# Kernel tuning notes

Hardware: AMD Instinct MI355X
Metric: run time of the kernel (lower is better)

The kernel has to match this reference:

```python
import jax, jax.numpy as jnp
import numpy as np

B, S, D, H = 4, 2048, 1024, 16
DK = D // H


def setup_inputs() -> dict:
    key = jax.random.key(0)
    ks = jax.random.split(key, 12)
    s = 1.0 / np.sqrt(D)
    return {
        "query": jax.random.normal(ks[0], (B, S, D), jnp.float32),
        "key": jax.random.normal(ks[1], (B, S, D), jnp.float32),
        "value": jax.random.normal(ks[2], (B, S, D), jnp.float32),
        "mask": jax.random.randint(ks[3], (B, S), 0, 2, jnp.int32),
        "wq": jax.random.normal(ks[4], (D, D), jnp.float32) * s,
        "bq": jnp.zeros((D,), jnp.float32),
        "wk": jax.random.normal(ks[5], (D, D), jnp.float32) * s,
        "bk": jnp.zeros((D,), jnp.float32),
        "wv": jax.random.normal(ks[6], (D, D), jnp.float32) * s,
        "bv": jnp.zeros((D,), jnp.float32),
        "wo": jax.random.normal(ks[7], (D, D), jnp.float32) * s,
        "bo": jnp.zeros((D,), jnp.float32),
    }


def reference(query, key, value, mask, wq, bq, wk, bk, wv, bv, wo, bo):
    # torch Linear: y = x @ W.T + b
    def proj(x, w, b):
        y = jnp.einsum('bsd,ed->bse', x, w) + b
        return y.reshape(B, S, H, DK).transpose(0, 2, 1, 3)  # [B,H,S,DK]

    q = proj(query, wq, bq)
    k = proj(key, wk, bk)
    v = proj(value, wv, bv)

    scores = jnp.einsum('bhqd,bhkd->bhqk', q, k) / jnp.sqrt(jnp.float32(DK))
    m = mask[:, None, None, :]  # [B,1,1,S_kv]
    scores = jnp.where(m == 0, jnp.float32(-1e9), scores)
    attn = jax.nn.softmax(scores, axis=-1)  # dropout p=0.0 (eval)
    out = jnp.einsum('bhqk,bhkd->bhqd', attn, v)
    out = out.transpose(0, 2, 1, 3).reshape(B, S, D)
    return jnp.einsum('bsd,ed->bse', out, wo) + bo
```

## Files before the change

kernel.cpp:

```cpp
#include <hip/hip_runtime.h>
#include <hip/hip_bf16.h>

typedef __bf16 bf16;
typedef bf16 bf16x2 __attribute__((ext_vector_type(2)));
typedef bf16 bf16x4 __attribute__((ext_vector_type(4)));
typedef bf16 bf16x8 __attribute__((ext_vector_type(8)));
typedef float f32x4 __attribute__((ext_vector_type(4)));
typedef float f32x16 __attribute__((ext_vector_type(16)));

#define MFMA16(A,B,C) __builtin_amdgcn_mfma_f32_16x16x32_bf16(A,B,C,0,0,0)
#define MFMA32(A,B,C) __builtin_amdgcn_mfma_f32_32x32x16_bf16(A,B,C,0,0,0)

__device__ __forceinline__ void gld_lds16(const void* g, void* l) {
  __builtin_amdgcn_global_load_lds(
      (const __attribute__((address_space(1))) void*)g,
      (__attribute__((address_space(3))) void*)l, 16, 0, 0);
}

__global__ void cast3_kernel(const float* __restrict__ s0, const float* __restrict__ s1,
                             const float* __restrict__ s2,
                             bf16* __restrict__ d0, bf16* __restrict__ d1, bf16* __restrict__ d2) {
  const int which = blockIdx.x >> 13;
  const int i = (blockIdx.x & 8191) * 256 + threadIdx.x;
  const float* s = which == 0 ? s0 : which == 1 ? s1 : s2;
  bf16* d = which == 0 ? d0 : which == 1 ? d1 : d2;
  float4 v = ((const float4*)s)[i];
  bf16x4 o;
  o[0] = (bf16)v.x; o[1] = (bf16)v.y; o[2] = (bf16)v.z; o[3] = (bf16)v.w;
  *(bf16x4*)(d + (size_t)i * 4) = o;
}

__global__ void cast4_kernel(const float* __restrict__ s0, const float* __restrict__ s1,
                             const float* __restrict__ s2, const float* __restrict__ s3,
                             bf16* __restrict__ d0, bf16* __restrict__ d1,
                             bf16* __restrict__ d2, bf16* __restrict__ d3) {
  const int which = blockIdx.x >> 10;
  const int i = (blockIdx.x & 1023) * 256 + threadIdx.x;
  const float* s = which == 0 ? s0 : which == 1 ? s1 : which == 2 ? s2 : s3;
  bf16* d = which == 0 ? d0 : which == 1 ? d1 : which == 2 ? d2 : d3;
  float4 v = ((const float4*)s)[i];
  bf16x4 o;
  o[0] = (bf16)v.x; o[1] = (bf16)v.y; o[2] = (bf16)v.z; o[3] = (bf16)v.w;
  *(bf16x4*)(d + (size_t)i * 4) = o;
}

template<int OUT_MODE>
__global__ __launch_bounds__(256) void gemm_bt_kernel(
    const bf16* __restrict__ A, const bf16* __restrict__ Bm,
    const float* __restrict__ bias, void* __restrict__ Cout,
    int M, int N, int K, float scale)
{
  __shared__ bf16 sA[2][128 * 32];
  __shared__ bf16 sB[2][128 * 32];
  const int t = threadIdx.x;
  const int lane = t & 63, w = t >> 6;
  const int wr = w >> 1, wc = w & 1;
  const int g = lane >> 4, c = lane & 15;
  const int bm = blockIdx.y, bn = blockIdx.x;

  f32x4 acc[4][4] = {};

  const int NT = K >> 5;
  const int arow = t >> 2;
  const int acol = (t & 3) * 8;
  const bf16* aBase = A + (size_t)(bm * 128) * K;
  const bf16* bBase = Bm + (size_t)(bn * 128) * K;

  auto stage = [&](int buf, int kt) {
    const int k0 = kt * 32;
#pragma unroll
    for (int i = 0; i < 2; ++i) {
      const int row = arow + i * 64;
      gld_lds16(aBase + (size_t)row * K + k0 + acol, &sA[buf][(i * 256 + t) * 8]);
      gld_lds16(bBase + (size_t)row * K + k0 + acol, &sB[buf][(i * 256 + t) * 8]);
    }
  };

  stage(0, 0);
  __syncthreads();
  int cur = 0;
  for (int kt = 0; kt < NT; ++kt) {
    if (kt + 1 < NT) stage(cur ^ 1, kt + 1);
    bf16x8 af[4], bfr[4];
#pragma unroll
    for (int m = 0; m < 4; ++m)
      af[m] = *(const bf16x8*)&sA[cur][(wr * 64 + m * 16 + c) * 32 + g * 8];
#pragma unroll
    for (int n = 0; n < 4; ++n)
      bfr[n] = *(const bf16x8*)&sB[cur][(wc * 64 + n * 16 + c) * 32 + g * 8];
    __builtin_amdgcn_s_setprio(1);
#pragma unroll
    for (int m = 0; m < 4; ++m)
#pragma unroll
      for (int n = 0; n < 4; ++n)
        acc[m][n] = MFMA16(af[m], bfr[n], acc[m][n]);
    __builtin_amdgcn_s_setprio(0);
    __syncthreads();
    cur ^= 1;
  }

#pragma unroll
  for (int n = 0; n < 4; ++n) {
    const int col = bn * 128 + wc * 64 + n * 16 + c;
    const float bv = bias[col];
#pragma unroll
    for (int m = 0; m < 4; ++m) {
#pragma unroll
      for (int r = 0; r < 4; ++r) {
        const int row = bm * 128 + wr * 64 + m * 16 + g * 4 + r;
        const float val = (acc[m][n][r] + bv) * scale;
        if (OUT_MODE == 0) {
          ((bf16*)Cout)[(size_t)row * N + col] = (bf16)val;
        } else if (OUT_MODE == 1) {
          const int bb = row >> 11, s = row & 2047;
          ((bf16*)Cout)[((size_t)(bb * 1024 + col)) * 2048 + s] = (bf16)val;
        } else {
          ((float*)Cout)[(size_t)row * N + col] = val;
        }
      }
    }
  }
}

__global__ __launch_bounds__(256) void attn_kernel(
    const bf16* __restrict__ Qp, const bf16* __restrict__ Kp, const bf16* __restrict__ Vt,
    const int* __restrict__ mask, bf16* __restrict__ Out)
{
  __shared__ bf16 sK[2][64 * 64];
  __shared__ bf16 sV[2][64 * 64];
  __shared__ bf16 sP[4][32 * 72];

  const int bh = blockIdx.x;
  const int b = bh >> 4, h = bh & 15;
  const int t = threadIdx.x, lane = t & 63, w = t >> 6;
  const int q32 = lane & 31, hi = lane >> 5;
  const int q0 = blockIdx.y * 128 + w * 32;

  const char* kBase = (const char*)(Kp + (size_t)(b * 2048) * 1024 + h * 64);
  const char* vBase = (const char*)(Vt + (size_t)(bh * 64) * 2048);

  auto stageKV = [&](int buf, int kt) {
#pragma unroll
    for (int i = 0; i < 2; ++i) {
      const int idx = i * 256 + t;
      const int row = idx >> 3;
      const int cb = ((t & 7) * 16) ^ ((row & 7) << 4);
      gld_lds16(kBase + (size_t)(kt * 64 + row) * 2048 + cb, (char*)sK[buf] + idx * 16);
      gld_lds16(vBase + (size_t)row * 4096 + kt * 128 + cb, (char*)sV[buf] + idx * 16);
    }
  };

  bf16x8 qf[4];
  const bf16* qrow = Qp + (size_t)(b * 2048 + q0 + q32) * 1024 + h * 64;
#pragma unroll
  for (int ks = 0; ks < 4; ++ks)
    qf[ks] = *(const bf16x8*)&qrow[ks * 16 + hi * 8];

  float mrun = -1e30f, lrun = 0.f;
  f32x16 aco[2] = {};

  const int* mrow = mask + b * 2048;
  bf16* pr = &sP[w][q32 * 72];

  stageKV(0, 0);
  __syncthreads();
  int cur = 0;
  for (int kt = 0; kt < 32; ++kt) {
    if (kt + 1 < 32) stageKV(cur ^ 1, kt + 1);

    f32x16 st[2] = {};
#pragma unroll
    for (int ks = 0; ks < 4; ++ks) {
      bf16x8 k0f, k1f;
      {
        const int row = q32;
        const int byt = (row * 128 + ks * 32 + hi * 16) ^ ((row & 7) << 4);
        k0f = *(const bf16x8*)((const char*)sK[cur] + byt);
      }
      {
        const int row = 32 + q32;
        const int byt = (row * 128 + ks * 32 + hi * 16) ^ ((row & 7) << 4);
        k1f = *(const bf16x8*)((const char*)sK[cur] + byt);
      }
      __builtin_amdgcn_s_setprio(1);
      st[0] = MFMA32(k0f, qf[ks], st[0]);
      st[1] = MFMA32(k1f, qf[ks], st[1]);
      __builtin_amdgcn_s_setprio(0);
    }

#pragma unroll
    for (int kf = 0; kf < 2; ++kf) {
#pragma unroll
      for (int q4 = 0; q4 < 4; ++q4) {
        const int4 mm = *(const int4*)&mrow[kt * 64 + kf * 32 + q4 * 8 + hi * 4];
        const int mv[4] = {mm.x, mm.y, mm.z, mm.w};
#pragma unroll
        for (int r4 = 0; r4 < 4; ++r4)
          st[kf][q4 * 4 + r4] += (mv[r4] == 0) ? -1e9f : 0.0f;
      }
    }

    float tmax = -1e30f;
#pragma unroll
    for (int i = 0; i < 16; ++i)
      tmax = fmaxf(tmax, fmaxf(st[0][i], st[1][i]));
    tmax = fmaxf(tmax, __shfl_xor(tmax, 32, 64));
    const float mnew = fmaxf(mrun, tmax);
    const float sc = exp2f(mrun - mnew);
    mrun = mnew;
    float rs = 0.f;
#pragma unroll
    for (int kf = 0; kf < 2; ++kf)
#pragma unroll
      for (int i = 0; i < 16; ++i) {
        const float p = exp2f(st[kf][i] - mnew);
        st[kf][i] = p;
        rs += p;
      }
    rs += __shfl_xor(rs, 32, 64);
    lrun = lrun * sc + rs;
    aco[0] *= sc;
    aco[1] *= sc;

#pragma unroll
    for (int kf = 0; kf < 2; ++kf)
#pragma unroll
      for (int j = 0; j < 8; ++j) {
        const int k = kf * 32 + (j >> 1) * 8 + hi * 4 + (j & 1) * 2;
        bf16x2 pv;
        pv[0] = (bf16)st[kf][2 * j];
        pv[1] = (bf16)st[kf][2 * j + 1];
        *(bf16x2*)&pr[k] = pv;
      }

    bf16x8 pa[4];
#pragma unroll
    for (int kk = 0; kk < 4; ++kk)
      pa[kk] = *(const bf16x8*)&sP[w][q32 * 72 + kk * 16 + hi * 8];
#pragma unroll
    for (int kk = 0; kk < 4; ++kk) {
      bf16x8 vb0, vb1;
      {
        const int row = q32;
        const int byt = (row * 128 + kk * 32 + hi * 16) ^ ((row & 7) << 4);
        vb0 = *(const bf16x8*)((const char*)sV[cur] + byt);
      }
      {
        const int row = 32 + q32;
        const int byt = (row * 128 + kk * 32 + hi * 16) ^ ((row & 7) << 4);
        vb1 = *(const bf16x8*)((const char*)sV[cur] + byt);
      }
      __builtin_amdgcn_s_setprio(1);
      aco[0] = MFMA32(vb0, pa[kk], aco[0]);
      aco[1] = MFMA32(vb1, pa[kk], aco[1]);
      __builtin_amdgcn_s_setprio(0);
    }

    __syncthreads();
    cur ^= 1;
  }

  const float inv = 1.0f / lrun;
  bf16* orow = Out + (size_t)(b * 2048 + q0 + q32) * 1024 + h * 64;
#pragma unroll
  for (int dkf = 0; dkf < 2; ++dkf)
#pragma unroll
    for (int q4 = 0; q4 < 4; ++q4) {
      bf16x4 o;
#pragma unroll
      for (int r4 = 0; r4 < 4; ++r4)
        o[r4] = (bf16)(aco[dkf][q4 * 4 + r4] * inv);
      *(bf16x4*)&orow[dkf * 32 + q4 * 8 + hi * 4] = o;
    }
}

extern "C" void kernel_launch(void* const* d_in, const int* in_sizes, int n_in,
                              void* d_out, int out_size, void* d_ws, size_t ws_size,
                              hipStream_t stream) {
  const float* q  = (const float*)d_in[0];
  const float* k  = (const float*)d_in[1];
  const float* v  = (const float*)d_in[2];
  const int*  msk = (const int*)d_in[3];
  const float* wq = (const float*)d_in[4];
  const float* bq = (const float*)d_in[5];
  const float* wk = (const float*)d_in[6];
  const float* bk = (const float*)d_in[7];
  const float* wv = (const float*)d_in[8];
  const float* bv = (const float*)d_in[9];
  const float* wo = (const float*)d_in[10];
  const float* bo = (const float*)d_in[11];

  bf16* ws = (bf16*)d_ws;
  const size_t NEL = 8192ull * 1024ull;
  bf16* qx  = ws;
  bf16* kx  = ws + NEL;
  bf16* vx  = ws + 2 * NEL;
  bf16* wqb = ws + 3 * NEL;
  bf16* wkb = wqb + 1048576;
  bf16* wvb = wkb + 1048576;
  bf16* wob = wvb + 1048576;
  bf16* qp  = wob + 1048576;
  bf16* kp  = qp + NEL;
  bf16* vt  = kp + NEL;
  bf16* ao  = vx;

  cast3_kernel<<<24576, 256, 0, stream>>>(q, k, v, qx, kx, vx);
  cast4_kernel<<<4096, 256, 0, stream>>>(wq, wk, wv, wo, wqb, wkb, wvb, wob);

  const float qscale = 0.125f * 1.44269504088896f;
  dim3 gg(8, 64);
  gemm_bt_kernel<0><<<gg, 256, 0, stream>>>(qx, wqb, bq, qp, 8192, 1024, 1024, qscale);
  gemm_bt_kernel<0><<<gg, 256, 0, stream>>>(kx, wkb, bk, kp, 8192, 1024, 1024, 1.0f);
  gemm_bt_kernel<1><<<gg, 256, 0, stream>>>(vx, wvb, bv, vt, 8192, 1024, 1024, 1.0f);
  attn_kernel<<<dim3(64, 16), 256, 0, stream>>>(qp, kp, vt, msk, ao);
  gemm_bt_kernel<2><<<gg, 256, 0, stream>>>(ao, wob, bo, d_out, 8192, 1024, 1024, 1.0f);
}
```

Baseline: 478.9 us.

## Keep softmax probabilities in registers via permlane swap; lazy rescale; preload mask bias

Replaces the LDS round-trip for the P tile with packed bf16 conversion and v_permlane32_swap to build the MFMA A operand directly in registers. It also initializes the score accumulator with the mask bias so the MFMA adds it, skips the running-max rescale when no new max exceeds the old one by a threshold, and splits the max and sum reductions into independent chains for more ILP. Together these remove LDS traffic and some per-tile VALU work, at the cost of inline asm that depends on the gfx950 ISA and a small numerical deviation from the deferred rescale.

```diff
diff --git a/kernel.cpp b/kernel.cpp
--- a/kernel.cpp
+++ b/kernel.cpp
@@ -7,6 +7,8 @@
 typedef bf16 bf16x8 __attribute__((ext_vector_type(8)));
 typedef float f32x4 __attribute__((ext_vector_type(4)));
 typedef float f32x16 __attribute__((ext_vector_type(16)));
+typedef unsigned int u32;
+typedef u32 u32x4 __attribute__((ext_vector_type(4)));
 
 #define MFMA16(A,B,C) __builtin_amdgcn_mfma_f32_16x16x32_bf16(A,B,C,0,0,0)
 #define MFMA32(A,B,C) __builtin_amdgcn_mfma_f32_32x32x16_bf16(A,B,C,0,0,0)
@@ -128,7 +130,6 @@
 {
   __shared__ bf16 sK[2][64 * 64];
   __shared__ bf16 sV[2][64 * 64];
-  __shared__ bf16 sP[4][32 * 72];
 
   const int bh = blockIdx.x;
   const int b = bh >> 4, h = bh & 15;
@@ -160,7 +161,6 @@
   f32x16 aco[2] = {};
 
   const int* mrow = mask + b * 2048;
-  bf16* pr = &sP[w][q32 * 72];
 
   stageKV(0, 0);
   __syncthreads();
@@ -168,7 +168,18 @@
   for (int kt = 0; kt < 32; ++kt) {
     if (kt + 1 < 32) stageKV(cur ^ 1, kt + 1);
 
-    f32x16 st[2] = {};
+    f32x16 st[2];
+#pragma unroll
+    for (int kf = 0; kf < 2; ++kf)
+#pragma unroll
+      for (int q4 = 0; q4 < 4; ++q4) {
+        const int4 mm = *(const int4*)&mrow[kt * 64 + kf * 32 + q4 * 8 + hi * 4];
+        st[kf][q4 * 4 + 0] = mm.x ? 0.0f : -1e9f;
+        st[kf][q4 * 4 + 1] = mm.y ? 0.0f : -1e9f;
+        st[kf][q4 * 4 + 2] = mm.z ? 0.0f : -1e9f;
+        st[kf][q4 * 4 + 3] = mm.w ? 0.0f : -1e9f;
+      }
+
 #pragma unroll
     for (int ks = 0; ks < 4; ++ks) {
       bf16x8 k0f, k1f;
@@ -188,55 +199,66 @@
       __builtin_amdgcn_s_setprio(0);
     }
 
+    float t0 = fmaxf(st[0][0], st[0][1]), t1 = fmaxf(st[0][2], st[0][3]);
+    float t2 = fmaxf(st[1][0], st[1][1]), t3 = fmaxf(st[1][2], st[1][3]);
+#pragma unroll
+    for (int i = 4; i < 16; i += 4) {
+      t0 = fmaxf(t0, fmaxf(st[0][i], st[0][i + 1]));
+      t1 = fmaxf(t1, fmaxf(st[0][i + 2], st[0][i + 3]));
+      t2 = fmaxf(t2, fmaxf(st[1][i], st[1][i + 1]));
+      t3 = fmaxf(t3, fmaxf(st[1][i + 2], st[1][i + 3]));
+    }
+    float tmax = fmaxf(fmaxf(t0, t1), fmaxf(t2, t3));
+    tmax = fmaxf(tmax, __shfl_xor(tmax, 32, 64));
+    if (!__all(tmax <= mrun + 11.5f)) {
+      const float mnew = fmaxf(mrun, tmax);
+      const float sc = exp2f(mrun - mnew);
+      mrun = mnew;
+      lrun *= sc;
+      aco[0] *= sc;
+      aco[1] *= sc;
+    }
+    float rs0 = 0.f, rs1 = 0.f, rs2 = 0.f, rs3 = 0.f;
+#pragma unroll
+    for (int i = 0; i < 16; i += 4) {
+      float p00 = exp2f(st[0][i] - mrun),     p01 = exp2f(st[0][i + 1] - mrun);
+      float p02 = exp2f(st[0][i + 2] - mrun), p03 = exp2f(st[0][i + 3] - mrun);
+      float p10 = exp2f(st[1][i] - mrun),     p11 = exp2f(st[1][i + 1] - mrun);
+      float p12 = exp2f(st[1][i + 2] - mrun), p13 = exp2f(st[1][i + 3] - mrun);
+      st[0][i] = p00; st[0][i + 1] = p01; st[0][i + 2] = p02; st[0][i + 3] = p03;
+      st[1][i] = p10; st[1][i + 1] = p11; st[1][i + 2] = p12; st[1][i + 3] = p13;
+      rs0 += p00 + p01; rs1 += p02 + p03;
+      rs2 += p10 + p11; rs3 += p12 + p13;
+    }
+    float rs = (rs0 + rs1) + (rs2 + rs3);
+    rs += __shfl_xor(rs, 32, 64);
+    lrun += rs;
+
+    bf16x8 pa[4];
 #pragma unroll
     for (int kf = 0; kf < 2; ++kf) {
-#pragma unroll
-      for (int q4 = 0; q4 < 4; ++q4) {
-        const int4 mm = *(const int4*)&mrow[kt * 64 + kf * 32 + q4 * 8 + hi * 4];
-        const int mv[4] = {mm.x, mm.y, mm.z, mm.w};
-#pragma unroll
-        for (int r4 = 0; r4 < 4; ++r4)
-          st[kf][q4 * 4 + r4] += (mv[r4] == 0) ? -1e9f : 0.0f;
-      }
-    }
-
-    float tmax = -1e30f;
-#pragma unroll
-    for (int i = 0; i < 16; ++i)
-      tmax = fmaxf(tmax, fmaxf(st[0][i], st[1][i]));
-    tmax = fmaxf(tmax, __shfl_xor(tmax, 32, 64));
-    const float mnew = fmaxf(mrun, tmax);
-    const float sc = exp2f(mrun - mnew);
-    mrun = mnew;
-    float rs = 0.f;
-#pragma unroll
-    for (int kf = 0; kf < 2; ++kf)
-#pragma unroll
-      for (int i = 0; i < 16; ++i) {
-        const float p = exp2f(st[kf][i] - mnew);
-        st[kf][i] = p;
-        rs += p;
-      }
-    rs += __shfl_xor(rs, 32, 64);
-    lrun = lrun * sc + rs;
-    aco[0] *= sc;
-    aco[1] *= sc;
-
-#pragma unroll
-    for (int kf = 0; kf < 2; ++kf)
-#pragma unroll
-      for (int j = 0; j < 8; ++j) {
-        const int k = kf * 32 + (j >> 1) * 8 + hi * 4 + (j & 1) * 2;
-        bf16x2 pv;
-        pv[0] = (bf16)st[kf][2 * j];
-        pv[1] = (bf16)st[kf][2 * j + 1];
-        *(bf16x2*)&pr[k] = pv;
-      }
-
-    bf16x8 pa[4];
-#pragma unroll
-    for (int kk = 0; kk < 4; ++kk)
-      pa[kk] = *(const bf16x8*)&sP[w][q32 * 72 + kk * 16 + hi * 8];
+      u32 u[4][2];
+#pragma unroll
+      for (int g2 = 0; g2 < 4; ++g2) {
+        asm("v_cvt_pk_bf16_f32 %0, %1, %2"
+            : "=v"(u[g2][0]) : "v"(st[kf][4 * g2 + 0]), "v"(st[kf][4 * g2 + 1]));
+        asm("v_cvt_pk_bf16_f32 %0, %1, %2"
+            : "=v"(u[g2][1]) : "v"(st[kf][4 * g2 + 2]), "v"(st[kf][4 * g2 + 3]));
+      }
+      u32 d0 = u[0][0], d2 = u[1][0];
+      asm("v_permlane32_swap_b32 %0, %1" : "+v"(d0), "+v"(d2));
+      u32 d1 = u[0][1], d3 = u[1][1];
+      asm("v_permlane32_swap_b32 %0, %1" : "+v"(d1), "+v"(d3));
+      u32x4 ud = {d0, d1, d2, d3};
+      pa[2 * kf] = __builtin_bit_cast(bf16x8, ud);
+      u32 e0 = u[2][0], e2 = u[3][0];
+      asm("v_permlane32_swap_b32 %0, %1" : "+v"(e0), "+v"(e2));
+      u32 e1 = u[2][1], e3 = u[3][1];
+      asm("v_permlane32_swap_b32 %0, %1" : "+v"(e1), "+v"(e3));
+      u32x4 ue = {e0, e1, e2, e3};
+      pa[2 * kf + 1] = __builtin_bit_cast(bf16x8, ue);
+    }
+
 #pragma unroll
     for (int kk = 0; kk < 4; ++kk) {
       bf16x8 vb0, vb1;
```

Result: faster. 448.0 us (-6.5%).
